# Optimization experiments

Hardware: AMD Instinct MI355X
Metric: run time of the kernel (lower is better)

Reference implementation:

```python
import jax, jax.numpy as jnp
import numpy as np

B, N, K, E = 2, 131072, 20, 256  # batch, points, n_slot, feat/embed dim
GN_GROUPS = 4
IOU_THR = 0.5
SCORE_THR = 0.04
TEMP = 0.05


def setup_inputs() -> dict:
    key = jax.random.key(0)
    ks = jax.random.split(key, 6)
    wscale = 1.0 / np.sqrt(E)
    return {
        "features": jax.random.normal(ks[0], (B, N, E), jnp.float32),
        "slots": jax.random.normal(ks[1], (B, K, E), jnp.float32),
        "w1": jax.random.normal(ks[2], (E, E), jnp.float32) * wscale,
        "b1": jax.random.normal(ks[3], (E,), jnp.float32) * 0.01,
        "gn_g": jnp.ones((E,), jnp.float32),
        "gn_b": jnp.zeros((E,), jnp.float32),
        "w2": jax.random.normal(ks[4], (E, E), jnp.float32) * wscale,
        "b2": jax.random.normal(ks[5], (E,), jnp.float32) * 0.01,
    }


def _l2norm(x, axis):
    n = jnp.linalg.norm(x, axis=axis, keepdims=True)
    return x / jnp.maximum(n, 1e-12)  # F.normalize semantics


def _nms_filter(mask):
    # mask: [N, K] soft instance probabilities (rows sum to 1)
    scores = mask.mean(axis=0)                       # [K]
    valid = scores >= SCORE_THR
    order = jnp.argsort(-scores)                     # descending score
    sm = mask[:, order]                              # [N, K] sorted columns
    bm = (sm > 0.5).astype(mask.dtype).T             # [K, N] binary masks
    areas = bm.sum(axis=1)                           # [K]
    inter = bm @ bm.T                                # [K, K] pairwise intersections
    union = areas[:, None] + areas[None, :] - inter
    iou = inter / (union + 1e-8)
    idx = jnp.arange(K)
    sup0 = ~valid[order]                             # invalid slots pre-suppressed

    def body(i, sup):
        keep_i = ~sup[i]
        return sup | (keep_i & (iou[i] > IOU_THR) & (idx > i))

    sup = jax.lax.fori_loop(0, K, body, sup0)
    kept = ~sup                                      # [K]
    # kept columns are packed (in score order) into the left of the output;
    # dropped columns are routed to a dump column K which is sliced away.
    pos = jnp.cumsum(kept) - 1
    cols = jnp.where(kept, pos, K)
    out = jnp.zeros((mask.shape[0], K + 1), mask.dtype).at[:, cols].set(sm)
    out = out[:, :K]
    # per-point renormalization over kept masks (zeros stay zero if none kept)
    return out / (out.sum(axis=1, keepdims=True) + 1e-8)


def reference(features, slots, w1, b1, gn_g, gn_b, w2, b2):
    # object_mlp: Conv1d(1x1) -> GroupNorm(4) -> ReLU -> Conv1d(1x1)
    x = jnp.einsum('bke,oe->bok', slots, w1) + b1[None, :, None]   # [B, E, K]
    xg = x.reshape(B, GN_GROUPS, E // GN_GROUPS, K)
    mu = xg.mean(axis=(2, 3), keepdims=True)
    var = xg.var(axis=(2, 3), keepdims=True)
    xg = (xg - mu) * jax.lax.rsqrt(var + 1e-5)
    x = xg.reshape(B, E, K) * gn_g[None, :, None] + gn_b[None, :, None]
    x = jax.nn.relu(x)
    slot = jnp.einsum('bek,fe->bfk', x, w2) + b2[None, :, None]    # [B, F=E, K]

    fn = _l2norm(features, axis=-1)                                # [B, N, E]
    sn = _l2norm(slot, axis=1)                                     # [B, E, K]
    logits = jnp.einsum('bnd,bdk->bnk', fn, sn) / TEMP
    mask = jax.nn.softmax(logits, axis=-1)                         # [B, N, K]

    out = jax.vmap(_nms_filter)(mask)                              # [B, N, K]
    return out.transpose(0, 2, 1)                                  # [B, K, N]
```

## Files before the change

kernel.cpp:

```cpp
#include <hip/hip_runtime.h>

#define B_ 2
#define N_ 131072
#define K_ 20
#define E_ 256
#define TEMP_ 0.05f
#define SCORE_THR_ 0.04f

#define WS_SCORE 0
#define WS_XN    1024
#define WS_SN    16384
#define WS_MASK  32768
#define WS_SPART 6291456

__device__ inline float wave_sum(float v) {
    #pragma unroll
    for (int off = 32; off; off >>= 1) v += __shfl_xor(v, off, 64);
    return v;
}

__global__ __launch_bounds__(256) void kA1(const float* __restrict__ slots,
                                           const float* __restrict__ w1,
                                           const float* __restrict__ b1,
                                           const float* __restrict__ gn_g,
                                           const float* __restrict__ gn_b,
                                           float* __restrict__ ws) {
    __shared__ __align__(16) float slds[20 * 260];
    __shared__ float red[2];
    const int t = threadIdx.x;
    const int b = blockIdx.x >> 2, g = blockIdx.x & 3;
    if (t < 2) red[t] = 0.f;
    const float* sb = slots + (size_t)b * K_ * E_;
    #pragma unroll
    for (int i = 0; i < 20; ++i) slds[i * 260 + t] = sb[i * 256 + t];
    __syncthreads();

    const int c = t >> 2, q = t & 3;
    const int o = g * 64 + c;
    const float* w1r = w1 + (size_t)o * E_;
    float acc[5] = {0.f, 0.f, 0.f, 0.f, 0.f};
    for (int e4 = 0; e4 < 64; ++e4) {
        const float4 w4 = *(const float4*)(w1r + e4 * 4);
        #pragma unroll
        for (int kk = 0; kk < 5; ++kk) {
            const float4 s4 = *(const float4*)&slds[(q * 5 + kk) * 260 + e4 * 4];
            acc[kk] += w4.x * s4.x + w4.y * s4.y + w4.z * s4.z + w4.w * s4.w;
        }
    }
    const float bias = b1[o];
    float s1 = 0.f, s2 = 0.f;
    #pragma unroll
    for (int kk = 0; kk < 5; ++kk) {
        acc[kk] += bias;
        s1 += acc[kk];
        s2 += acc[kk] * acc[kk];
    }
    s1 = wave_sum(s1);
    s2 = wave_sum(s2);
    if ((t & 63) == 0) { atomicAdd(&red[0], s1); atomicAdd(&red[1], s2); }
    __syncthreads();
    const float mean = red[0] * (1.f / 1280.f);
    const float var  = red[1] * (1.f / 1280.f) - mean * mean;
    const float rstd = rsqrtf(var + 1e-5f);
    const float gg = gn_g[o], gb = gn_b[o];
    float* xn = ws + WS_XN + (size_t)b * K_ * E_;
    #pragma unroll
    for (int kk = 0; kk < 5; ++kk) {
        float v = (acc[kk] - mean) * rstd * gg + gb;
        v = v > 0.f ? v : 0.f;
        xn[(q * 5 + kk) * 256 + o] = v;
    }
}

__global__ __launch_bounds__(256) void kA2(const float* __restrict__ w2,
                                           const float* __restrict__ b2,
                                           float* __restrict__ ws) {
    __shared__ __align__(16) float xv[256];
    __shared__ float wred[4];
    const int t = threadIdx.x;
    const int b = blockIdx.x / 20, k = blockIdx.x % 20;
    const float* xn = ws + WS_XN + (size_t)(b * 20 + k) * 256;
    xv[t] = xn[t];
    __syncthreads();
    const float* w2r = w2 + (size_t)t * 256;
    float acc = 0.f;
    for (int e4 = 0; e4 < 64; ++e4) {
        const float4 w4 = *(const float4*)(w2r + e4 * 4);
        const float4 x4 = *(const float4*)&xv[e4 * 4];
        acc += w4.x * x4.x + w4.y * x4.y + w4.z * x4.z + w4.w * x4.w;
    }
    acc += b2[t];
    float sq = wave_sum(acc * acc);
    if ((t & 63) == 0) wred[t >> 6] = sq;
    __syncthreads();
    const float nsq = wred[0] + wred[1] + wred[2] + wred[3];
    const float inv = 1.f / fmaxf(sqrtf(nsq), 1e-12f);
    ws[WS_SN + (size_t)(b * 20 + k) * 256 + t] = acc * inv;
}

__global__ __launch_bounds__(256, 2) void kB(const float* __restrict__ feat,
                                             float* __restrict__ ws) {
    __shared__ __align__(16) float snl[20 * 260];
    __shared__ __align__(16) float fl[32 * 260];
    __shared__ float pl[640];
    __shared__ float wsum[4][20];
    const int t = threadIdx.x;
    const int b = blockIdx.x >> 9;
    const int n0 = (blockIdx.x & 511) << 8;
    const float* sng = ws + WS_SN + (size_t)b * 5120;
    #pragma unroll
    for (int i = 0; i < 20; ++i) snl[i * 260 + t] = sng[i * 256 + t];
    const int p = t >> 3, s = t & 7;
    const int lane = t & 63, w = t >> 6;
    float sreg0 = 0.f, sreg1 = 0.f, sreg2 = 0.f;
    const float4* gbase = (const float4*)(feat + ((size_t)b * N_ + n0) * E_);
    float* mgbase = ws + WS_MASK + (size_t)b * 20 * N_ + n0;
    __syncthreads();

    for (int c = 0; c < 8; ++c) {
        const float4* g4 = gbase + (size_t)c * 2048;
        #pragma unroll
        for (int i = 0; i < 8; ++i) {
            const int idx = t + (i << 8);
            const float4 v = g4[idx];
            const int pp = idx >> 6, cc = idx & 63;
            *(float4*)&fl[pp * 260 + (cc << 2)] = v;
        }
        __syncthreads();
        float acc[20];
        float nr = 0.f;
        #pragma unroll
        for (int k = 0; k < 20; ++k) acc[k] = 0.f;
        const float* frow = &fl[p * 260];
        #pragma unroll
        for (int j = 0; j < 8; ++j) {
            const int col = (s << 2) + (j << 5);
            const float4 f4 = *(const float4*)&frow[col];
            nr += f4.x * f4.x + f4.y * f4.y + f4.z * f4.z + f4.w * f4.w;
            #pragma unroll
            for (int k = 0; k < 20; ++k) {
                const float4 s4 = *(const float4*)&snl[k * 260 + col];
                acc[k] += f4.x * s4.x + f4.y * s4.y + f4.z * s4.z + f4.w * s4.w;
            }
        }
        #pragma unroll
        for (int off = 1; off < 8; off <<= 1) {
            nr += __shfl_xor(nr, off, 64);
            #pragma unroll
            for (int k = 0; k < 20; ++k) acc[k] += __shfl_xor(acc[k], off, 64);
        }
        const float scl = rsqrtf(fmaxf(nr, 1e-24f)) * (1.f / TEMP_);
        float m = -1e30f;
        #pragma unroll
        for (int k = 0; k < 20; ++k) { acc[k] *= scl; m = fmaxf(m, acc[k]); }
        float su = 0.f;
        #pragma unroll
        for (int k = 0; k < 20; ++k) { acc[k] = __expf(acc[k] - m); su += acc[k]; }
        const float r = 1.f / su;
        float v0 = 0.f, v1 = 0.f, v2 = 0.f;
        #pragma unroll
        for (int k = 0; k < 8; ++k) {
            if (s == k) {
                v0 = acc[k] * r;
                v1 = acc[k + 8] * r;
                v2 = (k < 4) ? acc[k + 16] * r : 0.f;
            }
        }
        pl[(s << 5) + p] = v0;
        pl[((s + 8) << 5) + p] = v1;
        if (s < 4) pl[((s + 16) << 5) + p] = v2;
        sreg0 += v0; sreg1 += v1; sreg2 += v2;
        __syncthreads();
        #pragma unroll
        for (int i = 0; i < 3; ++i) {
            const int idx = t + (i << 8);
            if (idx < 640) {
                const int k = idx >> 5, pp = idx & 31;
                mgbase[(size_t)k * N_ + (c << 5) + pp] = pl[idx];
            }
        }
        __syncthreads();
    }
    #pragma unroll
    for (int off = 8; off < 64; off <<= 1) {
        sreg0 += __shfl_xor(sreg0, off, 64);
        sreg1 += __shfl_xor(sreg1, off, 64);
        sreg2 += __shfl_xor(sreg2, off, 64);
    }
    if (lane < 8) {
        wsum[w][lane] = sreg0;
        wsum[w][lane + 8] = sreg1;
        if (lane < 4) wsum[w][lane + 16] = sreg2;
    }
    __syncthreads();
    if (t < 20) {
        const float sum = wsum[0][t] + wsum[1][t] + wsum[2][t] + wsum[3][t];
        ws[WS_SPART + (size_t)blockIdx.x * 20 + t] = sum;
    }
}

__global__ __launch_bounds__(64) void kC(float* __restrict__ ws) {
    const int l = threadIdx.x;
    const int b = blockIdx.x / 20, k = blockIdx.x % 20;
    const float* sp = ws + WS_SPART;
    float sum = 0.f;
    #pragma unroll
    for (int i = 0; i < 8; ++i)
        sum += sp[(size_t)(b * 512 + l + i * 64) * 20 + k];
    sum = wave_sum(sum);
    if (l == 0) ws[WS_SCORE + blockIdx.x] = sum * (1.f / (float)N_);
}

__global__ __launch_bounds__(256) void kD(const float* __restrict__ ws,
                                          float* __restrict__ out) {
    __shared__ float sc[20];
    __shared__ int rnk[20];
    __shared__ int src[20];
    __shared__ int nk_s;
    const int t = threadIdx.x;
    const int b = blockIdx.x >> 9;
    const int n = (blockIdx.x & 511) * 256 + t;
    if (t < 20) sc[t] = ws[WS_SCORE + b * 20 + t];
    if (t == 0) nk_s = 0;
    __syncthreads();
    if (t < 20) {
        const float mys = sc[t];
        int rank = 0;
        for (int j = 0; j < 20; ++j) {
            const float o = sc[j];
            rank += (o > mys) || (o == mys && j < t);
        }
        rnk[t] = rank;
    }
    __syncthreads();
    if (t < 20 && sc[t] >= SCORE_THR_) {
        int pos = 0;
        for (int j = 0; j < 20; ++j)
            pos += (sc[j] >= SCORE_THR_) && (rnk[j] < rnk[t]);
        src[pos] = t;
        atomicAdd(&nk_s, 1);
    }
    __syncthreads();
    const int nk = nk_s;
    const float* mg = ws + WS_MASK + (size_t)b * 20 * N_;
    float mv[20];
    float den = 1e-8f;
    #pragma unroll
    for (int p = 0; p < 20; ++p) {
        float v = 0.f;
        if (p < nk) v = mg[(size_t)src[p] * N_ + n];
        mv[p] = v;
        den += v;
    }
    const float r = 1.f / den;
    float* og = out + (size_t)b * 20 * N_ + n;
    #pragma unroll
    for (int p = 0; p < 20; ++p) og[(size_t)p * N_] = (p < nk) ? mv[p] * r : 0.f;
}

extern "C" void kernel_launch(void* const* d_in, const int* in_sizes, int n_in,
                              void* d_out, int out_size, void* d_ws, size_t ws_size,
                              hipStream_t stream) {
    const float* feat  = (const float*)d_in[0];
    const float* slots = (const float*)d_in[1];
    const float* w1    = (const float*)d_in[2];
    const float* b1    = (const float*)d_in[3];
    const float* gng   = (const float*)d_in[4];
    const float* gnb   = (const float*)d_in[5];
    const float* w2    = (const float*)d_in[6];
    const float* b2    = (const float*)d_in[7];
    float* ws  = (float*)d_ws;
    float* out = (float*)d_out;

    kA1<<<8,    256, 0, stream>>>(slots, w1, b1, gng, gnb, ws);
    kA2<<<40,   256, 0, stream>>>(w2, b2, ws);
    kB <<<1024, 256, 0, stream>>>(feat, ws);
    kC <<<40,   64,  0, stream>>>(ws);
    kD <<<1024, 256, 0, stream>>>(ws, out);
}
```

Baseline: 431.9 us.

## Compute feature-slot logits with split-bf16 MFMA instead of FP32 FMA loops

Rewrites the main logits kernel to use 16x16x32 bf16 MFMA instructions. Each fp32 operand is split into a high and a low bf16 part, and three products (hi*hi, hi*lo, lo*hi) are accumulated to keep close to fp32 accuracy. Features are loaded straight from global memory into registers, so the LDS staging buffer and most block barriers go away. Softmax reduction now runs across MFMA lanes with shuffles, and mask rows are written directly as float4. The aim is to cut the FP32 ALU-bound dot-product cost; the trade-offs are conversion overhead and slightly lower precision near the 0.5 NMS threshold.

```diff
diff --git a/kernel.cpp b/kernel.cpp
--- a/kernel.cpp
+++ b/kernel.cpp
@@ -13,10 +13,26 @@
 #define WS_MASK  32768
 #define WS_SPART 6291456
 
+typedef __attribute__((ext_vector_type(8))) short short8;
+typedef __attribute__((ext_vector_type(4))) float f32x4;
+
 __device__ inline float wave_sum(float v) {
     #pragma unroll
     for (int off = 32; off; off >>= 1) v += __shfl_xor(v, off, 64);
     return v;
+}
+
+__device__ inline void cvt_hilo(const float4 a, const float4 b, short8& h, short8& l) {
+    float f[8] = {a.x, a.y, a.z, a.w, b.x, b.y, b.z, b.w};
+    #pragma unroll
+    for (int j = 0; j < 8; ++j) {
+        const unsigned u  = __float_as_uint(f[j]);
+        const unsigned hb = (u + 0x7fffu + ((u >> 16) & 1u)) & 0xffff0000u;
+        h[j] = (short)(hb >> 16);
+        const float r = f[j] - __uint_as_float(hb);
+        const unsigned v = __float_as_uint(r);
+        l[j] = (short)((v + 0x7fffu + ((v >> 16) & 1u)) >> 16);
+    }
 }
 
 __global__ __launch_bounds__(256) void kA1(const float* __restrict__ slots,
@@ -100,103 +116,105 @@
 
 __global__ __launch_bounds__(256, 2) void kB(const float* __restrict__ feat,
                                              float* __restrict__ ws) {
-    __shared__ __align__(16) float snl[20 * 260];
-    __shared__ __align__(16) float fl[32 * 260];
-    __shared__ float pl[640];
+    __shared__ short8 sfh[2][8][64];
+    __shared__ short8 sfl[2][8][64];
     __shared__ float wsum[4][20];
     const int t = threadIdx.x;
-    const int b = blockIdx.x >> 9;
-    const int n0 = (blockIdx.x & 511) << 8;
-    const float* sng = ws + WS_SN + (size_t)b * 5120;
-    #pragma unroll
-    for (int i = 0; i < 20; ++i) snl[i * 260 + t] = sng[i * 256 + t];
-    const int p = t >> 3, s = t & 7;
     const int lane = t & 63, w = t >> 6;
-    float sreg0 = 0.f, sreg1 = 0.f, sreg2 = 0.f;
-    const float4* gbase = (const float4*)(feat + ((size_t)b * N_ + n0) * E_);
-    float* mgbase = ws + WS_MASK + (size_t)b * 20 * N_ + n0;
-    __syncthreads();
-
-    for (int c = 0; c < 8; ++c) {
-        const float4* g4 = gbase + (size_t)c * 2048;
-        #pragma unroll
-        for (int i = 0; i < 8; ++i) {
-            const int idx = t + (i << 8);
-            const float4 v = g4[idx];
-            const int pp = idx >> 6, cc = idx & 63;
-            *(float4*)&fl[pp * 260 + (cc << 2)] = v;
-        }
-        __syncthreads();
-        float acc[20];
+    const int b = blockIdx.x >> 9, blk = blockIdx.x & 511;
+    const int s = lane & 15, g = lane >> 4;
+
+    {
+        #pragma unroll
+        for (int i = 0; i < 4; ++i) {
+            const int combo = w * 4 + i;
+            const int tile = combo >> 3, ks = combo & 7;
+            const int slot = tile * 16 + s;
+            short8 h, l;
+            if (slot < K_) {
+                const float* snp = ws + WS_SN + ((size_t)(b * K_ + slot)) * E_
+                                 + ks * 32 + g * 8;
+                cvt_hilo(*(const float4*)snp, *(const float4*)(snp + 4), h, l);
+            } else {
+                #pragma unroll
+                for (int j = 0; j < 8; ++j) { h[j] = 0; l[j] = 0; }
+            }
+            sfh[tile][ks][lane] = h;
+            sfl[tile][ks][lane] = l;
+        }
+    }
+    __syncthreads();
+
+    const float* fp0 = feat + ((size_t)b * N_ + blk * 256 + s) * E_;
+    float sreg0 = 0.f, sreg1 = 0.f;
+
+    for (int it = 0; it < 4; ++it) {
+        const int pb = w * 64 + it * 16;
+        const float* fp = fp0 + (size_t)pb * E_;
+        f32x4 c0 = {0.f, 0.f, 0.f, 0.f};
+        f32x4 c1 = {0.f, 0.f, 0.f, 0.f};
         float nr = 0.f;
         #pragma unroll
-        for (int k = 0; k < 20; ++k) acc[k] = 0.f;
-        const float* frow = &fl[p * 260];
-        #pragma unroll
-        for (int j = 0; j < 8; ++j) {
-            const int col = (s << 2) + (j << 5);
-            const float4 f4 = *(const float4*)&frow[col];
-            nr += f4.x * f4.x + f4.y * f4.y + f4.z * f4.z + f4.w * f4.w;
+        for (int ks = 0; ks < 8; ++ks) {
+            const float* q = fp + ks * 32 + g * 8;
+            const float4 a  = *(const float4*)q;
+            const float4 bb = *(const float4*)(q + 4);
+            nr += a.x * a.x + a.y * a.y + a.z * a.z + a.w * a.w
+                + bb.x * bb.x + bb.y * bb.y + bb.z * bb.z + bb.w * bb.w;
+            short8 fh, fl;
+            cvt_hilo(a, bb, fh, fl);
+            const short8 sh0 = sfh[0][ks][lane], sl0 = sfl[0][ks][lane];
+            const short8 sh1 = sfh[1][ks][lane], sl1 = sfl[1][ks][lane];
+            c0 = __builtin_amdgcn_mfma_f32_16x16x32_bf16(fh, sh0, c0, 0, 0, 0);
+            c1 = __builtin_amdgcn_mfma_f32_16x16x32_bf16(fh, sh1, c1, 0, 0, 0);
+            c0 = __builtin_amdgcn_mfma_f32_16x16x32_bf16(fh, sl0, c0, 0, 0, 0);
+            c1 = __builtin_amdgcn_mfma_f32_16x16x32_bf16(fh, sl1, c1, 0, 0, 0);
+            c0 = __builtin_amdgcn_mfma_f32_16x16x32_bf16(fl, sh0, c0, 0, 0, 0);
+            c1 = __builtin_amdgcn_mfma_f32_16x16x32_bf16(fl, sh1, c1, 0, 0, 0);
+        }
+        nr += __shfl_xor(nr, 16, 64);
+        nr += __shfl_xor(nr, 32, 64);
+        const float scl = rsqrtf(fmaxf(nr, 1e-24f)) * (1.f / TEMP_);
+
+        float p0[4], p1[4];
+        #pragma unroll
+        for (int r = 0; r < 4; ++r) {
+            const float sr = __shfl(scl, 4 * g + r, 64);
+            const float x0 = c0[r] * sr;
+            const float x1 = c1[r] * sr;
+            float m = (s < 4) ? fmaxf(x0, x1) : x0;
             #pragma unroll
-            for (int k = 0; k < 20; ++k) {
-                const float4 s4 = *(const float4*)&snl[k * 260 + col];
-                acc[k] += f4.x * s4.x + f4.y * s4.y + f4.z * s4.z + f4.w * s4.w;
-            }
-        }
-        #pragma unroll
-        for (int off = 1; off < 8; off <<= 1) {
-            nr += __shfl_xor(nr, off, 64);
+            for (int off = 1; off < 16; off <<= 1) m = fmaxf(m, __shfl_xor(m, off, 64));
+            const float e0 = __expf(x0 - m);
+            const float e1 = (s < 4) ? __expf(x1 - m) : 0.f;
+            float su = e0 + e1;
             #pragma unroll
-            for (int k = 0; k < 20; ++k) acc[k] += __shfl_xor(acc[k], off, 64);
-        }
-        const float scl = rsqrtf(fmaxf(nr, 1e-24f)) * (1.f / TEMP_);
-        float m = -1e30f;
-        #pragma unroll
-        for (int k = 0; k < 20; ++k) { acc[k] *= scl; m = fmaxf(m, acc[k]); }
-        float su = 0.f;
-        #pragma unroll
-        for (int k = 0; k < 20; ++k) { acc[k] = __expf(acc[k] - m); su += acc[k]; }
-        const float r = 1.f / su;
-        float v0 = 0.f, v1 = 0.f, v2 = 0.f;
-        #pragma unroll
-        for (int k = 0; k < 8; ++k) {
-            if (s == k) {
-                v0 = acc[k] * r;
-                v1 = acc[k + 8] * r;
-                v2 = (k < 4) ? acc[k + 16] * r : 0.f;
-            }
-        }
-        pl[(s << 5) + p] = v0;
-        pl[((s + 8) << 5) + p] = v1;
-        if (s < 4) pl[((s + 16) << 5) + p] = v2;
-        sreg0 += v0; sreg1 += v1; sreg2 += v2;
-        __syncthreads();
-        #pragma unroll
-        for (int i = 0; i < 3; ++i) {
-            const int idx = t + (i << 8);
-            if (idx < 640) {
-                const int k = idx >> 5, pp = idx & 31;
-                mgbase[(size_t)k * N_ + (c << 5) + pp] = pl[idx];
-            }
-        }
-        __syncthreads();
-    }
-    #pragma unroll
-    for (int off = 8; off < 64; off <<= 1) {
-        sreg0 += __shfl_xor(sreg0, off, 64);
-        sreg1 += __shfl_xor(sreg1, off, 64);
-        sreg2 += __shfl_xor(sreg2, off, 64);
-    }
-    if (lane < 8) {
-        wsum[w][lane] = sreg0;
-        wsum[w][lane + 8] = sreg1;
-        if (lane < 4) wsum[w][lane + 16] = sreg2;
-    }
-    __syncthreads();
-    if (t < 20) {
-        const float sum = wsum[0][t] + wsum[1][t] + wsum[2][t] + wsum[3][t];
-        ws[WS_SPART + (size_t)blockIdx.x * 20 + t] = sum;
-    }
+            for (int off = 1; off < 16; off <<= 1) su += __shfl_xor(su, off, 64);
+            const float inv = 1.f / su;
+            p0[r] = e0 * inv;
+            p1[r] = e1 * inv;
+        }
+        const int col = blk * 256 + pb + 4 * g;
+        float* mrow = ws + WS_MASK + ((size_t)b * K_ + s) * N_ + col;
+        *(float4*)mrow = make_float4(p0[0], p0[1], p0[2], p0[3]);
+        sreg0 += p0[0] + p0[1] + p0[2] + p0[3];
+        if (s < 4) {
+            float* mrow1 = ws + WS_MASK + ((size_t)b * K_ + 16 + s) * N_ + col;
+            *(float4*)mrow1 = make_float4(p1[0], p1[1], p1[2], p1[3]);
+            sreg1 += p1[0] + p1[1] + p1[2] + p1[3];
+        }
+    }
+
+    sreg0 += __shfl_xor(sreg0, 16, 64);
+    sreg0 += __shfl_xor(sreg0, 32, 64);
+    sreg1 += __shfl_xor(sreg1, 16, 64);
+    sreg1 += __shfl_xor(sreg1, 32, 64);
+    if (lane < 16) wsum[w][lane] = sreg0;
+    if (lane < 4)  wsum[w][16 + lane] = sreg1;
+    __syncthreads();
+    if (t < 20)
+        ws[WS_SPART + (size_t)blockIdx.x * 20 + t] =
+            wsum[0][t] + wsum[1][t] + wsum[2][t] + wsum[3][t];
 }
 
 __global__ __launch_bounds__(64) void kC(float* __restrict__ ws) {
```

New measurement: 423.9 us. Within noise of the previous version (-1.9%).
